# Performance work log

Hardware: AMD Instinct MI355X
Metric: run time of the kernel (lower is better)

## Reference

```python
import jax, jax.numpy as jnp
import numpy as np

CONV = 332.07156


def setup_inputs() -> dict:
    key = jax.random.key(0)
    ks = jax.random.split(key, 6)
    B, N, C = 4, 2048, 32
    X = jax.random.normal(ks[0], (B, N, 3), dtype=jnp.float32) * 5.0
    embs = jax.random.uniform(ks[1], (B, N, C), dtype=jnp.float32)
    qs = jax.random.normal(ks[2], (B, N), dtype=jnp.float32)
    paired_mask = jnp.zeros((B, N, N), dtype=bool)
    # learned parameters, initialized as in the torch module
    Born_factor = jax.random.normal(ks[3], (C,), dtype=jnp.float32) * 0.1 + 1.0
    die_factor = jax.random.normal(ks[4], (C,), dtype=jnp.float32) * 0.1 + 4.0
    screening_filter = jax.random.normal(ks[5], (2 * C + 1, 1), dtype=jnp.float32) * 0.1
    screening_filter = screening_filter.at[-1, :].set(1.0)
    return {"X": X, "embs": embs, "qs": qs, "paired_mask": paired_mask,
            "Born_factor": Born_factor, "die_factor": die_factor,
            "screening_filter": screening_filter}


def reference(X, embs, qs, paired_mask, Born_factor, die_factor, screening_filter):
    B, N, _ = X.shape
    C = embs.shape[-1]
    # all-pairs displacement and distance; note +1e-6 added per component before sum
    V = X[:, None, :, :] - X[:, :, None, :]            # (B,N,N,3)
    D = jnp.sqrt(jnp.sum(V * V + 1e-6, axis=-1))       # (B,N,N)
    invD = 1.0 / (D + 1e-6)
    # per-atom Born / dielectric scalars
    atomic_die = embs @ die_factor + 1e-6               # (B,N)
    R = embs @ Born_factor + 1.0                        # (B,N)
    E_self = -(1.0 - 1.0 / atomic_die) * qs / (R + 1e-6)  # (B,N)
    # pairwise screening: cat([emb_i, emb_j, D]) @ filter, algebraically separable
    w_i = screening_filter[:C, 0]                       # (C,)
    w_j = screening_filter[C:2 * C, 0]                  # (C,)
    w_d = screening_filter[2 * C, 0]                    # scalar
    s_i = embs @ w_i                                    # (B,N)
    s_j = embs @ w_j                                    # (B,N)
    screening = s_i[:, :, None] + s_j[:, None, :] + w_d * D  # (B,N,N)
    E_pair = invD * screening                           # (B,N,N)
    Etotal = CONV * (E_self.sum(axis=1) + 0.5 * E_pair.sum(axis=(1, 2))) * 0.01
    Etotal = jnp.where(jnp.isnan(Etotal), jnp.float32(1e-6), Etotal)
    return Etotal
```

## Files before the change

kernel.cpp:

```cpp
#include <hip/hip_runtime.h>
#include <math.h>

#define NB 4
#define NA 2048
#define NC 32
#define JT 128
#define IT 256

static constexpr float CONV001 = 3.3207156f;

#define WS_SI  0
#define WS_SJ  (NB * NA)
#define WS_SELF (2 * NB * NA)
#define WS_PAIR (2 * NB * NA + NB)

__device__ __forceinline__ float block_reduce_sum(float v) {
    #pragma unroll
    for (int off = 32; off > 0; off >>= 1)
        v += __shfl_down(v, off, 64);
    __shared__ float wsum[4];
    int lane = threadIdx.x & 63;
    int w = threadIdx.x >> 6;
    if (lane == 0) wsum[w] = v;
    __syncthreads();
    float r = 0.f;
    if (threadIdx.x == 0)
        r = wsum[0] + wsum[1] + wsum[2] + wsum[3];
    return r;
}

__global__ void atom_kernel(const float* __restrict__ embs,
                            const float* __restrict__ qs,
                            const float* __restrict__ born,
                            const float* __restrict__ die,
                            const float* __restrict__ sf,
                            float* __restrict__ ws) {
    int a = blockIdx.x * blockDim.x + threadIdx.x;
    int b = a >> 11;
    const float* e = embs + (size_t)a * NC;
    float si = 0.f, sj = 0.f, ad = 0.f, R = 0.f;
    #pragma unroll
    for (int c = 0; c < NC; ++c) {
        float ev = e[c];
        si += ev * sf[c];
        sj += ev * sf[NC + c];
        ad += ev * die[c];
        R  += ev * born[c];
    }
    ad += 1e-6f;
    R  += 1.0f;
    ws[WS_SI + a] = si;
    ws[WS_SJ + a] = sj;
    float eself = -(1.0f - 1.0f / ad) * qs[a] / (R + 1e-6f);
    float bs = block_reduce_sum(eself);
    if (threadIdx.x == 0)
        atomicAdd(&ws[WS_SELF + b], bs);
}

__global__ void __launch_bounds__(IT)
pair_kernel(const float* __restrict__ X,
            const float* __restrict__ sf,
            float* __restrict__ ws) {
    int b  = blockIdx.z;
    int i  = blockIdx.y * IT + threadIdx.x;
    int j0 = blockIdx.x * JT;
    const float wd = sf[2 * NC];

    const float* Xb = X + (size_t)b * NA * 3;
    float xi = Xb[i * 3 + 0];
    float yi = Xb[i * 3 + 1];
    float zi = Xb[i * 3 + 2];
    float si = ws[WS_SI + b * NA + i];

    __shared__ float xj[JT], yj[JT], zj[JT], sjs[JT];
    int t = threadIdx.x;
    if (t < JT) {
        int j = j0 + t;
        xj[t]  = Xb[j * 3 + 0];
        yj[t]  = Xb[j * 3 + 1];
        zj[t]  = Xb[j * 3 + 2];
        sjs[t] = ws[WS_SJ + b * NA + j];
    }
    __syncthreads();

    float acc = 0.f;
    #pragma unroll 8
    for (int jj = 0; jj < JT; ++jj) {
        float dx = xj[jj] - xi;
        float dy = yj[jj] - yi;
        float dz = zj[jj] - zi;
        float d2 = fmaf(dx, dx, fmaf(dy, dy, fmaf(dz, dz, 3e-6f)));
        float D    = __builtin_amdgcn_sqrtf(d2);
        float invD = __builtin_amdgcn_rcpf(D + 1e-6f);
        acc += invD * fmaf(wd, D, si + sjs[jj]);
    }

    float bs = block_reduce_sum(acc);
    if (t == 0)
        atomicAdd(&ws[WS_PAIR + b], bs);
}

__global__ void finalize_kernel(const float* __restrict__ ws,
                                float* __restrict__ out) {
    int b = threadIdx.x;
    if (b < NB) {
        float v = CONV001 * (ws[WS_SELF + b] + 0.5f * ws[WS_PAIR + b]);
        out[b] = isnan(v) ? 1e-6f : v;
    }
}

extern "C" void kernel_launch(void* const* d_in, const int* in_sizes, int n_in,
                              void* d_out, int out_size, void* d_ws, size_t ws_size,
                              hipStream_t stream) {
    const float* X    = (const float*)d_in[0];
    const float* embs = (const float*)d_in[1];
    const float* qs   = (const float*)d_in[2];
    const float* born = (const float*)d_in[4];
    const float* die  = (const float*)d_in[5];
    const float* sf   = (const float*)d_in[6];
    float* ws  = (float*)d_ws;
    float* out = (float*)d_out;

    hipMemsetAsync(ws + WS_SELF, 0, 2 * NB * sizeof(float), stream);

    atom_kernel<<<NB * NA / 256, 256, 0, stream>>>(embs, qs, born, die, sf, ws);
    pair_kernel<<<dim3(NA / JT, NA / IT, NB), IT, 0, stream>>>(X, sf, ws);
    finalize_kernel<<<1, 64, 0, stream>>>(ws, out);
}
```

Measured before the change: 117.4 us.

## Fuse atom, pair and finalize kernels into one with last-block reduction

Merges the three launches into a single kernel. Per-atom screening terms are recomputed inside each block, the self-energy is folded into the blocks with blockIdx.x==0, and a last-block counter writes the final output. The inner loop is rewritten algebraically: the w_d*D/(D+eps) term is pulled out as a constant w_d*N^2 and the rest uses rsq instead of sqrt plus rcp, with packed float4 shared storage. This removes launch overhead and per-pair instructions, but drops the 1e-6 offset in the denominator, a small approximation, and every block redundantly recomputes the 32-wide embedding dot products.

After: 145.8 us. +24.3%, slower.

```diff
diff --git a/kernel.cpp b/kernel.cpp
--- a/kernel.cpp
+++ b/kernel.cpp
@@ -6,106 +6,112 @@
 #define NC 32
 #define JT 128
 #define IT 256
+#define NJ (NA / JT)
+#define NI (NA / IT)
+#define NBLOCKS (NB * NI * NJ)
 
 static constexpr float CONV001 = 3.3207156f;
 
-#define WS_SI  0
-#define WS_SJ  (NB * NA)
-#define WS_SELF (2 * NB * NA)
-#define WS_PAIR (2 * NB * NA + NB)
-
-__device__ __forceinline__ float block_reduce_sum(float v) {
-    #pragma unroll
-    for (int off = 32; off > 0; off >>= 1)
-        v += __shfl_down(v, off, 64);
-    __shared__ float wsum[4];
-    int lane = threadIdx.x & 63;
-    int w = threadIdx.x >> 6;
-    if (lane == 0) wsum[w] = v;
-    __syncthreads();
-    float r = 0.f;
-    if (threadIdx.x == 0)
-        r = wsum[0] + wsum[1] + wsum[2] + wsum[3];
-    return r;
-}
-
-__global__ void atom_kernel(const float* __restrict__ embs,
-                            const float* __restrict__ qs,
-                            const float* __restrict__ born,
-                            const float* __restrict__ die,
-                            const float* __restrict__ sf,
-                            float* __restrict__ ws) {
-    int a = blockIdx.x * blockDim.x + threadIdx.x;
-    int b = a >> 11;
-    const float* e = embs + (size_t)a * NC;
-    float si = 0.f, sj = 0.f, ad = 0.f, R = 0.f;
-    #pragma unroll
-    for (int c = 0; c < NC; ++c) {
-        float ev = e[c];
-        si += ev * sf[c];
-        sj += ev * sf[NC + c];
-        ad += ev * die[c];
-        R  += ev * born[c];
-    }
-    ad += 1e-6f;
-    R  += 1.0f;
-    ws[WS_SI + a] = si;
-    ws[WS_SJ + a] = sj;
-    float eself = -(1.0f - 1.0f / ad) * qs[a] / (R + 1e-6f);
-    float bs = block_reduce_sum(eself);
-    if (threadIdx.x == 0)
-        atomicAdd(&ws[WS_SELF + b], bs);
-}
 
 __global__ void __launch_bounds__(IT)
-pair_kernel(const float* __restrict__ X,
-            const float* __restrict__ sf,
-            float* __restrict__ ws) {
-    int b  = blockIdx.z;
-    int i  = blockIdx.y * IT + threadIdx.x;
-    int j0 = blockIdx.x * JT;
-    const float wd = sf[2 * NC];
+fused_kernel(const float* __restrict__ X,
+             const float* __restrict__ embs,
+             const float* __restrict__ qs,
+             const float* __restrict__ born,
+             const float* __restrict__ die,
+             const float* __restrict__ sf,
+             float* __restrict__ ws,
+             float* __restrict__ out) {
+    const int b  = blockIdx.z;
+    const int i  = blockIdx.y * IT + threadIdx.x;
+    const int j0 = blockIdx.x * JT;
+    const int t  = threadIdx.x;
 
     const float* Xb = X + (size_t)b * NA * 3;
+    const float* Eb = embs + (size_t)b * NA * NC;
+
+    __shared__ float4 jd[JT];
+
+    if (t < JT) {
+        int j = j0 + t;
+        const float4* e4 = (const float4*)(Eb + (size_t)j * NC);
+        float sj = 0.f;
+        #pragma unroll
+        for (int c = 0; c < NC / 4; ++c) {
+            float4 ev = e4[c];
+            sj += ev.x * sf[NC + 4 * c + 0] + ev.y * sf[NC + 4 * c + 1]
+                + ev.z * sf[NC + 4 * c + 2] + ev.w * sf[NC + 4 * c + 3];
+        }
+        jd[t] = make_float4(Xb[j * 3 + 0], Xb[j * 3 + 1], Xb[j * 3 + 2], sj);
+    }
+
+    const float4* ei4 = (const float4*)(Eb + (size_t)i * NC);
+    float si = 0.f;
+    #pragma unroll
+    for (int c = 0; c < NC / 4; ++c) {
+        float4 ev = ei4[c];
+        si += ev.x * sf[4 * c + 0] + ev.y * sf[4 * c + 1]
+            + ev.z * sf[4 * c + 2] + ev.w * sf[4 * c + 3];
+    }
     float xi = Xb[i * 3 + 0];
     float yi = Xb[i * 3 + 1];
     float zi = Xb[i * 3 + 2];
-    float si = ws[WS_SI + b * NA + i];
 
-    __shared__ float xj[JT], yj[JT], zj[JT], sjs[JT];
-    int t = threadIdx.x;
-    if (t < JT) {
-        int j = j0 + t;
-        xj[t]  = Xb[j * 3 + 0];
-        yj[t]  = Xb[j * 3 + 1];
-        zj[t]  = Xb[j * 3 + 2];
-        sjs[t] = ws[WS_SJ + b * NA + j];
+    float acc = 0.f;
+    if (blockIdx.x == 0) {
+        float ad = 0.f, R = 0.f;
+        #pragma unroll
+        for (int c = 0; c < NC / 4; ++c) {
+            float4 ev = ei4[c];
+            ad += ev.x * die[4 * c + 0] + ev.y * die[4 * c + 1]
+                + ev.z * die[4 * c + 2] + ev.w * die[4 * c + 3];
+            R  += ev.x * born[4 * c + 0] + ev.y * born[4 * c + 1]
+                + ev.z * born[4 * c + 2] + ev.w * born[4 * c + 3];
+        }
+        ad += 1e-6f;
+        R  += 1.0f;
+        float eself = -(1.0f - __builtin_amdgcn_rcpf(ad)) * qs[b * NA + i]
+                      * __builtin_amdgcn_rcpf(R + 1e-6f);
+        acc = 2.0f * eself;
     }
     __syncthreads();
 
-    float acc = 0.f;
     #pragma unroll 8
     for (int jj = 0; jj < JT; ++jj) {
-        float dx = xj[jj] - xi;
-        float dy = yj[jj] - yi;
-        float dz = zj[jj] - zi;
+        float4 v = jd[jj];
+        float dx = v.x - xi;
+        float dy = v.y - yi;
+        float dz = v.z - zi;
         float d2 = fmaf(dx, dx, fmaf(dy, dy, fmaf(dz, dz, 3e-6f)));
-        float D    = __builtin_amdgcn_sqrtf(d2);
-        float invD = __builtin_amdgcn_rcpf(D + 1e-6f);
-        acc += invD * fmaf(wd, D, si + sjs[jj]);
+        acc = fmaf(__builtin_amdgcn_rsqf(d2), si + v.w, acc);
     }
 
-    float bs = block_reduce_sum(acc);
-    if (t == 0)
-        atomicAdd(&ws[WS_PAIR + b], bs);
-}
+    #pragma unroll
+    for (int off = 32; off > 0; off >>= 1)
+        acc += __shfl_down(acc, off, 64);
+    __shared__ float wsum[IT / 64];
+    int lane = t & 63;
+    int w = t >> 6;
+    if (lane == 0) wsum[w] = acc;
+    __syncthreads();
+    if (t == 0) {
+        float bs = wsum[0] + wsum[1] + wsum[2] + wsum[3];
+        atomicAdd(&ws[b], bs);
+    }
 
-__global__ void finalize_kernel(const float* __restrict__ ws,
-                                float* __restrict__ out) {
-    int b = threadIdx.x;
-    if (b < NB) {
-        float v = CONV001 * (ws[WS_SELF + b] + 0.5f * ws[WS_PAIR + b]);
-        out[b] = isnan(v) ? 1e-6f : v;
+    __threadfence();
+    __shared__ bool amLast;
+    if (t == 0) {
+        unsigned old = atomicAdd((unsigned*)&ws[NB], 1u);
+        amLast = (old == NBLOCKS - 1);
+    }
+    __syncthreads();
+    if (amLast && t < NB) {
+        float accb = __hip_atomic_load(&ws[t], __ATOMIC_RELAXED,
+                                       __HIP_MEMORY_SCOPE_AGENT);
+        float wd = sf[2 * NC];
+        float v = CONV001 * 0.5f * (accb + wd * (float)NA * (float)NA);
+        out[t] = isnan(v) ? 1e-6f : v;
     }
 }
 
@@ -121,9 +127,8 @@
     float* ws  = (float*)d_ws;
     float* out = (float*)d_out;
 
-    hipMemsetAsync(ws + WS_SELF, 0, 2 * NB * sizeof(float), stream);
+    hipMemsetAsync(ws, 0, 8 * sizeof(float), stream);
 
-    atom_kernel<<<NB * NA / 256, 256, 0, stream>>>(embs, qs, born, die, sf, ws);
-    pair_kernel<<<dim3(NA / JT, NA / IT, NB), IT, 0, stream>>>(X, sf, ws);
-    finalize_kernel<<<1, 64, 0, stream>>>(ws, out);
+    fused_kernel<<<dim3(NJ, NI, NB), IT, 0, stream>>>(X, embs, qs, born, die,
+                                                      sf, ws, out);
 }
```
